# Performance work log

Measured on AMD Instinct MI355X. Metric: run time of the kernel, lower is better.

The kernel has to match this reference:

```python
import jax, jax.numpy as jnp
import numpy as np

ALPHA = 4.0   # spikingjelly surrogate.Sigmoid default alpha
TAU = 2.0
HEADS = 8

@jax.custom_vjp
def spike_fn(x):
    return (x >= 0).astype(x.dtype)

def _spike_fwd(x):
    return spike_fn(x), x

def _spike_bwd(x, g):
    s = jax.nn.sigmoid(ALPHA * x)
    return (g * ALPHA * s * (1.0 - s),)

spike_fn.defvjp(_spike_fwd, _spike_bwd)

def lif(x, v_th=1.0):
    """Multi-step LIF over leading time axis. Hard reset to 0, detach_reset."""
    def step(v, xt):
        v = v + (xt - v) / TAU
        s = spike_fn(v - v_th)
        v = v * (1.0 - jax.lax.stop_gradient(s))
        return v, s
    _, spikes = jax.lax.scan(step, jnp.zeros_like(x[0]), x)
    return spikes

def conv1x1(x, w, b=None):
    # x: (T,B,C,H,W), w: (O,C) -> (T,B,O,H,W)
    y = jnp.einsum('tbchw,oc->tbohw', x, w)
    if b is not None:
        y = y + b[None, None, :, None, None]
    return y

def bn(x, gamma, beta, mean, var, eps=1e-5):
    inv = gamma / jnp.sqrt(var + eps)
    shift = beta - mean * inv
    return x * inv[None, None, :, None, None] + shift[None, None, :, None, None]

def setup_inputs() -> dict:
    key = jax.random.key(0)
    T, B, C, H, W = 4, 16, 512, 16, 16
    ks = jax.random.split(key, 24)
    def w(k):
        return jax.random.normal(k, (C, C), jnp.float32) * (1.0 / np.sqrt(C))
    def bn_params(k0, k1):
        g = 1.0 + 0.1 * jax.random.normal(k0, (C,), jnp.float32)
        b = 0.1 * jax.random.normal(k1, (C,), jnp.float32)
        m = 0.1 * jax.random.normal(jax.random.fold_in(k0, 7), (C,), jnp.float32)
        v = jax.random.uniform(jax.random.fold_in(k1, 7), (C,), jnp.float32, 0.5, 1.5)
        return g, b, m, v
    x = jax.random.normal(ks[0], (T, B, C, H, W), jnp.float32)
    q_g, q_b, q_m, q_v = bn_params(ks[4], ks[5])
    k_g, k_b, k_m, k_v = bn_params(ks[6], ks[7])
    v_g, v_b, v_m, v_v = bn_params(ks[8], ks[9])
    p_g, p_b2, p_m, p_v = bn_params(ks[10], ks[11])
    return {
        'x': x,
        'q_w': w(ks[1]), 'q_g': q_g, 'q_b': q_b, 'q_m': q_m, 'q_v': q_v,
        'k_w': w(ks[2]), 'k_g': k_g, 'k_b': k_b, 'k_m': k_m, 'k_v': k_v,
        'v_w': w(ks[3]), 'v_g': v_g, 'v_b': v_b, 'v_m': v_m, 'v_v': v_v,
        'proj_w': w(ks[12]),
        'proj_b': 0.1 * jax.random.normal(ks[13], (C,), jnp.float32),
        'p_g': p_g, 'p_b2': p_b2, 'p_m': p_m, 'p_v': p_v,
    }

def reference(x, q_w, q_g, q_b, q_m, q_v, k_w, k_g, k_b, k_m, k_v,
              v_w, v_g, v_b, v_m, v_v, proj_w, proj_b, p_g, p_b2, p_m, p_v):
    T, B, C, H, W = x.shape
    d = C // HEADS
    N = H * W
    identity = x
    xs = lif(x)  # shortcut_lif

    def to_heads(y):
        # (T,B,C,H,W) -> flatten(3) -> (T,B,C,N) -> (T,B,N,C) -> (T,B,N,h,d) -> (T,B,h,N,d)
        return y.reshape(T, B, C, N).transpose(0, 1, 3, 2).reshape(T, B, N, HEADS, d).transpose(0, 1, 3, 2, 4)

    q = to_heads(lif(bn(conv1x1(xs, q_w), q_g, q_b, q_m, q_v)))
    k = to_heads(lif(bn(conv1x1(xs, k_w), k_g, k_b, k_m, k_v)))
    v = to_heads(lif(bn(conv1x1(xs, v_w), v_g, v_b, v_m, v_v)))

    kv = (k * v).sum(axis=3, keepdims=True)        # (T,B,h,1,d) linear spike attention
    kv = lif(kv, v_th=0.5)                         # talking_heads_lif (conv1d never applied in source forward)
    attn = q * kv                                  # (T,B,h,N,d)

    y = attn.transpose(0, 1, 2, 4, 3).reshape(T, B, C, H, W)
    y = bn(conv1x1(y, proj_w, proj_b), p_g, p_b2, p_m, p_v)
    return y + identity
```

## Files before the change

kernel.cpp:

```cpp
#include <hip/hip_runtime.h>


#define T_  4
#define B_  16
#define C_  512
#define N_  256
#define O3_ 1536
#define EPS_ 1e-5f

typedef unsigned int uint32;

__global__ void k0_prep(const float* __restrict__ qw, const float* __restrict__ kw,
                        const float* __restrict__ vw, const float* __restrict__ pw,
                        const float* qg,const float* qb,const float* qm,const float* qv,
                        const float* kg,const float* kb,const float* km,const float* kvr,
                        const float* vg,const float* vb,const float* vm,const float* vv,
                        const float* pg,const float* pb2,const float* pm,const float* pv,
                        const float* projb,
                        float* __restrict__ wqkv_t, float* __restrict__ pwt,
                        float* __restrict__ bnc){
    __shared__ float tile[64 * 65];
    int bx = blockIdx.x, tid = threadIdx.x;
    if (bx < 256) {
        const float* src; float* dst; int ocol;
        int tl;
        if (bx < 192) { int g = bx / 64; tl = bx % 64;
            src = (g == 0) ? qw : (g == 1) ? kw : vw;
            dst = wqkv_t; ocol = g * 512;
        } else { tl = bx - 192; src = pw; dst = pwt; ocol = 0; }
        int o0 = (tl >> 3) * 64, c0 = (tl & 7) * 64;
        int dstride = (bx < 192) ? O3_ : C_;
        #pragma unroll
        for (int i = 0; i < 16; i++) {
            int idx = i * 256 + tid;
            int cl = idx & 63, ol = idx >> 6;
            tile[ol * 65 + cl] = src[(size_t)(o0 + ol) * C_ + c0 + cl];
        }
        __syncthreads();
        #pragma unroll
        for (int i = 0; i < 16; i++) {
            int idx = i * 256 + tid;
            int ol = idx & 63, cl = idx >> 6;
            dst[(size_t)(c0 + cl) * dstride + ocol + o0 + ol] = tile[ol * 65 + cl];
        }
    } else {
        int ch = (bx - 256) * 256 + tid;
        if (ch < C_) {
            {   float inv = qg[ch] / sqrtf(qv[ch] + EPS_);
                bnc[ch] = inv;            bnc[512 + ch]  = qb[ch] - qm[ch] * inv; }
            {   float inv = kg[ch] / sqrtf(kvr[ch] + EPS_);
                bnc[1024 + ch] = inv;     bnc[1536 + ch] = kb[ch] - km[ch] * inv; }
            {   float inv = vg[ch] / sqrtf(vv[ch] + EPS_);
                bnc[2048 + ch] = inv;     bnc[2560 + ch] = vb[ch] - vm[ch] * inv; }
            {   float inv = pg[ch] / sqrtf(pv[ch] + EPS_);
                float shift = pb2[ch] - pm[ch] * inv;
                bnc[3072 + ch] = inv;     bnc[3584 + ch] = projb[ch] * inv + shift; }
        }
    }
}

__global__ void k1_lif_x(const float* __restrict__ x, uint32* __restrict__ xs_mask32){
    __shared__ uint32 sm32[64 * 17];
    int b = blockIdx.x, c0 = blockIdx.y * 64, n0 = blockIdx.z * 64;
    int tid = threadIdx.x;
    #pragma unroll
    for (int i = 0; i < 4; i++) {
        int idx = i * 256 + tid;
        int nq = idx & 15, cl = idx >> 4;
        const float* xp = x + ((size_t)b * C_ + c0 + cl) * N_ + n0 + nq * 4;
        float4 xv[4];
        #pragma unroll
        for (int t = 0; t < 4; t++)
            xv[t] = *reinterpret_cast<const float4*>(xp + (size_t)t * B_ * C_ * N_);
        uint32 packed = 0;
        #pragma unroll
        for (int e = 0; e < 4; e++) {
            float v = 0.f; unsigned m = 0;
            #pragma unroll
            for (int t = 0; t < 4; t++) {
                float xt = reinterpret_cast<const float*>(&xv[t])[e];
                v = v + (xt - v) * 0.5f;
                if (v - 1.0f >= 0.f) { m |= 1u << t; v = 0.f; }
            }
            packed |= m << (8 * e);
        }
        sm32[cl * 17 + nq] = packed;
    }
    __syncthreads();
    #pragma unroll
    for (int i = 0; i < 4; i++) {
        int idx = i * 256 + tid;
        int cq = idx & 15, nl = idx >> 4;
        uint32 outp = 0;
        #pragma unroll
        for (int e = 0; e < 4; e++) {
            uint32 wv = sm32[(cq * 4 + e) * 17 + (nl >> 2)];
            outp |= ((wv >> (8 * (nl & 3))) & 0xffu) << (8 * e);
        }
        xs_mask32[((size_t)b * N_ + n0 + nl) * 128 + (c0 >> 2) + cq] = outp;
    }
}

__global__ __launch_bounds__(384) void
k2_qkv(const unsigned char* __restrict__ xs_mask,
       const float* __restrict__ wqkv_t,
       const float* __restrict__ bnc,
       unsigned char* __restrict__ q_mask,
       unsigned char* __restrict__ kvand_mask){
    __shared__ uint32 smask[128];
    __shared__ uint32 scnt;
    __shared__ uint32 slist[512];
    int n = blockIdx.x, b = blockIdx.y, tid = threadIdx.x;
    size_t colbase = ((size_t)b * N_ + n) * C_;
    if (tid < 128) smask[tid] = reinterpret_cast<const uint32*>(xs_mask + colbase)[tid];
    if (tid == 0) scnt = 0;
    __syncthreads();
    if (tid < 256) {
        const unsigned char* smb = (const unsigned char*)smask;
        #pragma unroll
        for (int h = 0; h < 2; h++) {
            int c = tid + (h << 8);
            unsigned m = smb[c];
            if (m) { unsigned p = atomicAdd(&scnt, 1u); slist[p] = (unsigned)c | (m << 16); }
        }
    }
    __syncthreads();
    int cnt = scnt;

    int g = tid >> 7;
    float acc[4][4];
    #pragma unroll
    for (int t = 0; t < 4; t++)
        #pragma unroll
        for (int i = 0; i < 4; i++) acc[t][i] = 0.f;

#define ACC4(t, w_) { acc[t][0]+=w_.x; acc[t][1]+=w_.y; acc[t][2]+=w_.z; acc[t][3]+=w_.w; }
    int j = 0;
    for (; j + 4 <= cnt; j += 4) {
        unsigned e0 = __builtin_amdgcn_readfirstlane(slist[j]);
        unsigned e1 = __builtin_amdgcn_readfirstlane(slist[j + 1]);
        unsigned e2 = __builtin_amdgcn_readfirstlane(slist[j + 2]);
        unsigned e3 = __builtin_amdgcn_readfirstlane(slist[j + 3]);
        float4 w0 = reinterpret_cast<const float4*>(wqkv_t + (size_t)(e0 & 0xffffu) * O3_)[tid];
        float4 w1 = reinterpret_cast<const float4*>(wqkv_t + (size_t)(e1 & 0xffffu) * O3_)[tid];
        float4 w2 = reinterpret_cast<const float4*>(wqkv_t + (size_t)(e2 & 0xffffu) * O3_)[tid];
        float4 w3 = reinterpret_cast<const float4*>(wqkv_t + (size_t)(e3 & 0xffffu) * O3_)[tid];
        unsigned m0 = e0 >> 16, m1 = e1 >> 16, m2 = e2 >> 16, m3 = e3 >> 16;
        if (m0 & 1u) ACC4(0, w0)  if (m0 & 2u) ACC4(1, w0)
        if (m0 & 4u) ACC4(2, w0)  if (m0 & 8u) ACC4(3, w0)
        if (m1 & 1u) ACC4(0, w1)  if (m1 & 2u) ACC4(1, w1)
        if (m1 & 4u) ACC4(2, w1)  if (m1 & 8u) ACC4(3, w1)
        if (m2 & 1u) ACC4(0, w2)  if (m2 & 2u) ACC4(1, w2)
        if (m2 & 4u) ACC4(2, w2)  if (m2 & 8u) ACC4(3, w2)
        if (m3 & 1u) ACC4(0, w3)  if (m3 & 2u) ACC4(1, w3)
        if (m3 & 4u) ACC4(2, w3)  if (m3 & 8u) ACC4(3, w3)
    }
    for (; j < cnt; j++) {
        unsigned e0 = __builtin_amdgcn_readfirstlane(slist[j]);
        float4 w0 = reinterpret_cast<const float4*>(wqkv_t + (size_t)(e0 & 0xffffu) * O3_)[tid];
        unsigned m0 = e0 >> 16;
        if (m0 & 1u) ACC4(0, w0)  if (m0 & 2u) ACC4(1, w0)
        if (m0 & 4u) ACC4(2, w0)  if (m0 & 8u) ACC4(3, w0)
    }
#undef ACC4

    int chb = (tid & 127) * 4;
    unsigned packed = 0;
    #pragma unroll
    for (int i = 0; i < 4; i++) {
        int ch = chb + i;
        float inv = bnc[g * 1024 + ch];
        float sh  = bnc[g * 1024 + 512 + ch];
        float v = 0.f; unsigned bits = 0;
        #pragma unroll
        for (int t = 0; t < 4; t++) {
            float pre = acc[t][i] * inv + sh;
            v = v + (pre - v) * 0.5f;
            if (v - 1.0f >= 0.f) { bits |= 1u << t; v = 0.f; }
        }
        packed |= bits << (8 * i);
    }
    if (g == 0)      reinterpret_cast<uint32*>(q_mask + colbase)[tid] = packed;
    else if (g == 1) smask[tid - 128] = packed;
    __syncthreads();
    if (g == 2) {
        unsigned kb = smask[tid - 256];
        reinterpret_cast<uint32*>(kvand_mask + colbase)[tid - 256] = packed & kb;
    }
}

__global__ void k3_kv(const uint32* __restrict__ kvand32,
                      unsigned char* __restrict__ kvs_mask){
    __shared__ uint32 part[4][128];
    int b = blockIdx.x, tid = threadIdx.x;
    int c4 = tid & 127, sub = tid >> 7;
    const uint32* p = kvand32 + (size_t)b * N_ * 128 + (size_t)sub * 128 * 128 + c4;
    uint32 cnt0 = 0, cnt1 = 0, cnt2 = 0, cnt3 = 0;
    for (int i = 0; i < 128; i++) {
        uint32 m = p[(size_t)i * 128];
        cnt0 +=  m        & 0x01010101u;
        cnt1 += (m >> 1)  & 0x01010101u;
        cnt2 += (m >> 2)  & 0x01010101u;
        cnt3 += (m >> 3)  & 0x01010101u;
    }
    if (sub == 1) { part[0][c4] = cnt0; part[1][c4] = cnt1; part[2][c4] = cnt2; part[3][c4] = cnt3; }
    __syncthreads();
    if (sub == 0) {
        uint32 o0 = part[0][c4], o1 = part[1][c4], o2 = part[2][c4], o3 = part[3][c4];
        unsigned outp = 0;
        #pragma unroll
        for (int e = 0; e < 4; e++) {
            int sh = 8 * e;
            float cn[4];
            cn[0] = (float)(int)(((cnt0 >> sh) & 0xffu) + ((o0 >> sh) & 0xffu));
            cn[1] = (float)(int)(((cnt1 >> sh) & 0xffu) + ((o1 >> sh) & 0xffu));
            cn[2] = (float)(int)(((cnt2 >> sh) & 0xffu) + ((o2 >> sh) & 0xffu));
            cn[3] = (float)(int)(((cnt3 >> sh) & 0xffu) + ((o3 >> sh) & 0xffu));
            float v = 0.f; unsigned bits = 0;
            #pragma unroll
            for (int t = 0; t < 4; t++) {
                v = v + (cn[t] - v) * 0.5f;
                if (v - 0.5f >= 0.f) { bits |= 1u << t; v = 0.f; }
            }
            outp |= bits << sh;
        }
        reinterpret_cast<uint32*>(kvs_mask + (size_t)b * C_)[c4] = outp;
    }
}

__global__ __launch_bounds__(256) void
k4_attn_proj(const unsigned char* __restrict__ q_mask,
             const unsigned char* __restrict__ kvs_mask,
             const float* __restrict__ pwt,
             const float* __restrict__ bnc,
             float* __restrict__ y_t){
    __shared__ uint32 smask[2][128];
    __shared__ uint32 scnt[2];
    __shared__ uint32 slist[2][512];
    int b = blockIdx.y, tid = threadIdx.x;
    int col = tid >> 7, ctid = tid & 127;
    int n = blockIdx.x * 2 + col;
    size_t colbase = ((size_t)b * N_ + n) * C_;
    {
        uint32 qm = reinterpret_cast<const uint32*>(q_mask + colbase)[ctid];
        uint32 kv = reinterpret_cast<const uint32*>(kvs_mask + (size_t)b * C_)[ctid];
        smask[col][ctid] = qm & kv;
    }
    if (ctid == 0) scnt[col] = 0;
    __syncthreads();
    {
        const unsigned char* smb = (const unsigned char*)smask[col];
        #pragma unroll
        for (int h = 0; h < 4; h++) {
            int c = ctid * 4 + h;
            unsigned m = smb[c];
            if (m) { unsigned p = atomicAdd(&scnt[col], 1u); slist[col][p] = (unsigned)c | (m << 16); }
        }
    }
    __syncthreads();
    int cnt = scnt[col];
    const uint32* lst = slist[col];

    float acc[4][4];
    #pragma unroll
    for (int t = 0; t < 4; t++)
        #pragma unroll
        for (int i = 0; i < 4; i++) acc[t][i] = 0.f;

#define ACC4(t, w_) { acc[t][0]+=w_.x; acc[t][1]+=w_.y; acc[t][2]+=w_.z; acc[t][3]+=w_.w; }
    int j = 0;
    for (; j + 4 <= cnt; j += 4) {
        unsigned e0 = __builtin_amdgcn_readfirstlane(lst[j]);
        unsigned e1 = __builtin_amdgcn_readfirstlane(lst[j + 1]);
        unsigned e2 = __builtin_amdgcn_readfirstlane(lst[j + 2]);
        unsigned e3 = __builtin_amdgcn_readfirstlane(lst[j + 3]);
        float4 w0 = reinterpret_cast<const float4*>(pwt + (size_t)(e0 & 0xffffu) * C_)[ctid];
        float4 w1 = reinterpret_cast<const float4*>(pwt + (size_t)(e1 & 0xffffu) * C_)[ctid];
        float4 w2 = reinterpret_cast<const float4*>(pwt + (size_t)(e2 & 0xffffu) * C_)[ctid];
        float4 w3 = reinterpret_cast<const float4*>(pwt + (size_t)(e3 & 0xffffu) * C_)[ctid];
        unsigned m0 = e0 >> 16, m1 = e1 >> 16, m2 = e2 >> 16, m3 = e3 >> 16;
        if (m0 & 1u) ACC4(0, w0)  if (m0 & 2u) ACC4(1, w0)
        if (m0 & 4u) ACC4(2, w0)  if (m0 & 8u) ACC4(3, w0)
        if (m1 & 1u) ACC4(0, w1)  if (m1 & 2u) ACC4(1, w1)
        if (m1 & 4u) ACC4(2, w1)  if (m1 & 8u) ACC4(3, w1)
        if (m2 & 1u) ACC4(0, w2)  if (m2 & 2u) ACC4(1, w2)
        if (m2 & 4u) ACC4(2, w2)  if (m2 & 8u) ACC4(3, w2)
        if (m3 & 1u) ACC4(0, w3)  if (m3 & 2u) ACC4(1, w3)
        if (m3 & 4u) ACC4(2, w3)  if (m3 & 8u) ACC4(3, w3)
    }
    for (; j < cnt; j++) {
        unsigned e0 = __builtin_amdgcn_readfirstlane(lst[j]);
        float4 w0 = reinterpret_cast<const float4*>(pwt + (size_t)(e0 & 0xffffu) * C_)[ctid];
        unsigned m0 = e0 >> 16;
        if (m0 & 1u) ACC4(0, w0)  if (m0 & 2u) ACC4(1, w0)
        if (m0 & 4u) ACC4(2, w0)  if (m0 & 8u) ACC4(3, w0)
    }
#undef ACC4

    float4 inv = reinterpret_cast<const float4*>(bnc + 3072)[ctid];
    float4 sh  = reinterpret_cast<const float4*>(bnc + 3584)[ctid];
    #pragma unroll
    for (int t = 0; t < 4; t++) {
        float4 y4;
        y4.x = acc[t][0] * inv.x + sh.x;
        y4.y = acc[t][1] * inv.y + sh.y;
        y4.z = acc[t][2] * inv.z + sh.z;
        y4.w = acc[t][3] * inv.w + sh.w;
        reinterpret_cast<float4*>(y_t + (((size_t)t * B_ + b) * N_ + n) * C_)[ctid] = y4;
    }
}

__global__ void k5_out(const float* __restrict__ y_t, const float* __restrict__ x,
                       float* __restrict__ out){
    __shared__ float tile[64 * 65];
    int b = blockIdx.x, o0 = blockIdx.y * 64, n0 = blockIdx.z * 64;
    int tid = threadIdx.x;
    for (int t = 0; t < T_; t++) {
        __syncthreads();
        #pragma unroll
        for (int i = 0; i < 4; i++) {
            int idx = i * 256 + tid;
            int o4 = idx & 15, nl = idx >> 4;
            float4 yv = *reinterpret_cast<const float4*>(
                y_t + (((size_t)t * B_ + b) * N_ + n0 + nl) * C_ + o0 + o4 * 4);
            tile[(o4 * 4 + 0) * 65 + nl] = yv.x;
            tile[(o4 * 4 + 1) * 65 + nl] = yv.y;
            tile[(o4 * 4 + 2) * 65 + nl] = yv.z;
            tile[(o4 * 4 + 3) * 65 + nl] = yv.w;
        }
        __syncthreads();
        #pragma unroll
        for (int i = 0; i < 4; i++) {
            int idx = i * 256 + tid;
            int n4 = idx & 15, ol = idx >> 4;
            size_t a = (((size_t)t * B_ + b) * C_ + o0 + ol) * N_ + n0 + n4 * 4;
            float4 xv = *reinterpret_cast<const float4*>(x + a);
            float4 yv;
            yv.x = tile[ol * 65 + n4 * 4 + 0] + xv.x;
            yv.y = tile[ol * 65 + n4 * 4 + 1] + xv.y;
            yv.z = tile[ol * 65 + n4 * 4 + 2] + xv.z;
            yv.w = tile[ol * 65 + n4 * 4 + 3] + xv.w;
            *reinterpret_cast<float4*>(out + a) = yv;
        }
    }
}

extern "C" void kernel_launch(void* const* d_in, const int* in_sizes, int n_in,
                              void* d_out, int out_size, void* d_ws, size_t ws_size,
                              hipStream_t stream){
    const float* x     = (const float*)d_in[0];
    const float* q_w   = (const float*)d_in[1];
    const float* q_g   = (const float*)d_in[2];
    const float* q_b   = (const float*)d_in[3];
    const float* q_m   = (const float*)d_in[4];
    const float* q_v   = (const float*)d_in[5];
    const float* k_w   = (const float*)d_in[6];
    const float* k_g   = (const float*)d_in[7];
    const float* k_b   = (const float*)d_in[8];
    const float* k_m   = (const float*)d_in[9];
    const float* k_v   = (const float*)d_in[10];
    const float* v_w   = (const float*)d_in[11];
    const float* v_g   = (const float*)d_in[12];
    const float* v_b   = (const float*)d_in[13];
    const float* v_m   = (const float*)d_in[14];
    const float* v_v   = (const float*)d_in[15];
    const float* pr_w  = (const float*)d_in[16];
    const float* pr_b  = (const float*)d_in[17];
    const float* p_g   = (const float*)d_in[18];
    const float* p_b2  = (const float*)d_in[19];
    const float* p_m   = (const float*)d_in[20];
    const float* p_v   = (const float*)d_in[21];
    float* out = (float*)d_out;

    char* ws = (char*)d_ws;
    float* wqkv_t          = (float*)(ws + 0);
    float* pwt             = (float*)(ws + 3145728);
    float* bnc             = (float*)(ws + 4194304);
    unsigned char* xs_mask = (unsigned char*)(ws + 4210688);
    unsigned char* q_mask  = (unsigned char*)(ws + 6307840);
    unsigned char* kvand   = (unsigned char*)(ws + 8404992);
    unsigned char* kvs     = (unsigned char*)(ws + 10502144);
    float* y_t             = (float*)(ws + 10510336);

    hipLaunchKernelGGL(k0_prep, dim3(258), dim3(256), 0, stream,
                       q_w, k_w, v_w, pr_w,
                       q_g,q_b,q_m,q_v, k_g,k_b,k_m,k_v, v_g,v_b,v_m,v_v,
                       p_g,p_b2,p_m,p_v, pr_b, wqkv_t, pwt, bnc);
    hipLaunchKernelGGL(k1_lif_x, dim3(B_, C_/64, N_/64), dim3(256), 0, stream,
                       x, (uint32*)xs_mask);
    hipLaunchKernelGGL(k2_qkv, dim3(N_, B_), dim3(384), 0, stream,
                       xs_mask, wqkv_t, bnc, q_mask, kvand);
    hipLaunchKernelGGL(k3_kv, dim3(B_), dim3(256), 0, stream,
                       (const uint32*)kvand, kvs);
    hipLaunchKernelGGL(k4_attn_proj, dim3(N_/2, B_), dim3(256), 0, stream,
                       q_mask, kvs, pwt, bnc, y_t);
    hipLaunchKernelGGL(k5_out, dim3(B_, C_/64, N_/64), dim3(256), 0, stream, y_t, x, out);
}
```

Before: 212.4 us.

## Fold LIF-x into prep kernel and replace kv reduction kernel with atomics

Merges the input-LIF spike packing into the weight-prep kernel and adds blocks that zero a per-batch count buffer. The separate k3 reduction over the k&v spike masks is removed. k2 now atomically accumulates packed 16-bit per-channel counts into global memory, and k4 recomputes the talking-heads LIF from those counts. This cuts two launches and the round trip of the kvand mask, at the cost of global atomic contention in k2 and redundant LIF work in every k4 block.

```diff
diff --git a/kernel.cpp b/kernel.cpp
--- a/kernel.cpp
+++ b/kernel.cpp
@@ -10,16 +10,18 @@
 
 typedef unsigned int uint32;
 
-__global__ void k0_prep(const float* __restrict__ qw, const float* __restrict__ kw,
-                        const float* __restrict__ vw, const float* __restrict__ pw,
-                        const float* qg,const float* qb,const float* qm,const float* qv,
-                        const float* kg,const float* kb,const float* km,const float* kvr,
-                        const float* vg,const float* vb,const float* vm,const float* vv,
-                        const float* pg,const float* pb2,const float* pm,const float* pv,
-                        const float* projb,
-                        float* __restrict__ wqkv_t, float* __restrict__ pwt,
-                        float* __restrict__ bnc){
+__global__ void k_prep(const float* __restrict__ qw, const float* __restrict__ kw,
+                       const float* __restrict__ vw, const float* __restrict__ pw,
+                       const float* qg,const float* qb,const float* qm,const float* qv,
+                       const float* kg,const float* kb,const float* km,const float* kvr,
+                       const float* vg,const float* vb,const float* vm,const float* vv,
+                       const float* pg,const float* pb2,const float* pm,const float* pv,
+                       const float* projb, const float* __restrict__ x,
+                       float* __restrict__ wqkv_t, float* __restrict__ pwt,
+                       float* __restrict__ bnc, uint32* __restrict__ xs_mask32,
+                       uint32* __restrict__ cnt32){
     __shared__ float tile[64 * 65];
+    __shared__ uint32 sm32[64 * 17];
     int bx = blockIdx.x, tid = threadIdx.x;
     if (bx < 256) {
         const float* src; float* dst; int ocol;
@@ -43,7 +45,7 @@
             int ol = idx & 63, cl = idx >> 6;
             dst[(size_t)(c0 + cl) * dstride + ocol + o0 + ol] = tile[ol * 65 + cl];
         }
-    } else {
+    } else if (bx < 258) {
         int ch = (bx - 256) * 256 + tid;
         if (ch < C_) {
             {   float inv = qg[ch] / sqrtf(qv[ch] + EPS_);
@@ -56,48 +58,49 @@
                 float shift = pb2[ch] - pm[ch] * inv;
                 bnc[3072 + ch] = inv;     bnc[3584 + ch] = projb[ch] * inv + shift; }
         }
-    }
-}
-
-__global__ void k1_lif_x(const float* __restrict__ x, uint32* __restrict__ xs_mask32){
-    __shared__ uint32 sm32[64 * 17];
-    int b = blockIdx.x, c0 = blockIdx.y * 64, n0 = blockIdx.z * 64;
-    int tid = threadIdx.x;
-    #pragma unroll
-    for (int i = 0; i < 4; i++) {
-        int idx = i * 256 + tid;
-        int nq = idx & 15, cl = idx >> 4;
-        const float* xp = x + ((size_t)b * C_ + c0 + cl) * N_ + n0 + nq * 4;
-        float4 xv[4];
-        #pragma unroll
-        for (int t = 0; t < 4; t++)
-            xv[t] = *reinterpret_cast<const float4*>(xp + (size_t)t * B_ * C_ * N_);
-        uint32 packed = 0;
-        #pragma unroll
-        for (int e = 0; e < 4; e++) {
-            float v = 0.f; unsigned m = 0;
-            #pragma unroll
-            for (int t = 0; t < 4; t++) {
-                float xt = reinterpret_cast<const float*>(&xv[t])[e];
-                v = v + (xt - v) * 0.5f;
-                if (v - 1.0f >= 0.f) { m |= 1u << t; v = 0.f; }
+    } else if (bx < 770) {
+        int r = bx - 258;
+        int b = r >> 5, rem = r & 31;
+        int c0 = (rem >> 2) * 64, n0 = (rem & 3) * 64;
+        #pragma unroll
+        for (int i = 0; i < 4; i++) {
+            int idx = i * 256 + tid;
+            int nq = idx & 15, cl = idx >> 4;
+            const float* xp = x + ((size_t)b * C_ + c0 + cl) * N_ + n0 + nq * 4;
+            float4 xv[4];
+            #pragma unroll
+            for (int t = 0; t < 4; t++)
+                xv[t] = *reinterpret_cast<const float4*>(xp + (size_t)t * B_ * C_ * N_);
+            uint32 packed = 0;
+            #pragma unroll
+            for (int e = 0; e < 4; e++) {
+                float v = 0.f; unsigned m = 0;
+                #pragma unroll
+                for (int t = 0; t < 4; t++) {
+                    float xt = reinterpret_cast<const float*>(&xv[t])[e];
+                    v = v + (xt - v) * 0.5f;
+                    if (v - 1.0f >= 0.f) { m |= 1u << t; v = 0.f; }
+                }
+                packed |= m << (8 * e);
             }
-            packed |= m << (8 * e);
-        }
-        sm32[cl * 17 + nq] = packed;
-    }
-    __syncthreads();
-    #pragma unroll
-    for (int i = 0; i < 4; i++) {
-        int idx = i * 256 + tid;
-        int cq = idx & 15, nl = idx >> 4;
-        uint32 outp = 0;
-        #pragma unroll
-        for (int e = 0; e < 4; e++) {
-            uint32 wv = sm32[(cq * 4 + e) * 17 + (nl >> 2)];
-            outp |= ((wv >> (8 * (nl & 3))) & 0xffu) << (8 * e);
-        }
-        xs_mask32[((size_t)b * N_ + n0 + nl) * 128 + (c0 >> 2) + cq] = outp;
+            sm32[cl * 17 + nq] = packed;
+        }
+        __syncthreads();
+        #pragma unroll
+        for (int i = 0; i < 4; i++) {
+            int idx = i * 256 + tid;
+            int cq = idx & 15, nl = idx >> 4;
+            uint32 outp = 0;
+            #pragma unroll
+            for (int e = 0; e < 4; e++) {
+                uint32 wv = sm32[(cq * 4 + e) * 17 + (nl >> 2)];
+                outp |= ((wv >> (8 * (nl & 3))) & 0xffu) << (8 * e);
+            }
+            xs_mask32[((size_t)b * N_ + n0 + nl) * 128 + (c0 >> 2) + cq] = outp;
+        }
+    } else {
+        int idx = (bx - 770) * 256 + tid;
+        cnt32[idx] = 0;
     }
 }
 
@@ -106,7 +109,7 @@
        const float* __restrict__ wqkv_t,
        const float* __restrict__ bnc,
        unsigned char* __restrict__ q_mask,
-       unsigned char* __restrict__ kvand_mask){
+       uint32* __restrict__ cnt32){
     __shared__ uint32 smask[128];
     __shared__ uint32 scnt;
     __shared__ uint32 slist[512];
@@ -185,52 +188,23 @@
     __syncthreads();
     if (g == 2) {
         unsigned kb = smask[tid - 256];
-        reinterpret_cast<uint32*>(kvand_mask + colbase)[tid - 256] = packed & kb;
-    }
-}
-
-__global__ void k3_kv(const uint32* __restrict__ kvand32,
-                      unsigned char* __restrict__ kvs_mask){
-    __shared__ uint32 part[4][128];
-    int b = blockIdx.x, tid = threadIdx.x;
-    int c4 = tid & 127, sub = tid >> 7;
-    const uint32* p = kvand32 + (size_t)b * N_ * 128 + (size_t)sub * 128 * 128 + c4;
-    uint32 cnt0 = 0, cnt1 = 0, cnt2 = 0, cnt3 = 0;
-    for (int i = 0; i < 128; i++) {
-        uint32 m = p[(size_t)i * 128];
-        cnt0 +=  m        & 0x01010101u;
-        cnt1 += (m >> 1)  & 0x01010101u;
-        cnt2 += (m >> 2)  & 0x01010101u;
-        cnt3 += (m >> 3)  & 0x01010101u;
-    }
-    if (sub == 1) { part[0][c4] = cnt0; part[1][c4] = cnt1; part[2][c4] = cnt2; part[3][c4] = cnt3; }
-    __syncthreads();
-    if (sub == 0) {
-        uint32 o0 = part[0][c4], o1 = part[1][c4], o2 = part[2][c4], o3 = part[3][c4];
-        unsigned outp = 0;
-        #pragma unroll
-        for (int e = 0; e < 4; e++) {
-            int sh = 8 * e;
-            float cn[4];
-            cn[0] = (float)(int)(((cnt0 >> sh) & 0xffu) + ((o0 >> sh) & 0xffu));
-            cn[1] = (float)(int)(((cnt1 >> sh) & 0xffu) + ((o1 >> sh) & 0xffu));
-            cn[2] = (float)(int)(((cnt2 >> sh) & 0xffu) + ((o2 >> sh) & 0xffu));
-            cn[3] = (float)(int)(((cnt3 >> sh) & 0xffu) + ((o3 >> sh) & 0xffu));
-            float v = 0.f; unsigned bits = 0;
+        unsigned kv = packed & kb;
+        if (kv) {
+            uint32* cbase = cnt32 + b * 1024 + (chb >> 1);
             #pragma unroll
             for (int t = 0; t < 4; t++) {
-                v = v + (cn[t] - v) * 0.5f;
-                if (v - 0.5f >= 0.f) { bits |= 1u << t; v = 0.f; }
+                unsigned v01 = ((kv >> t) & 1u) | (((kv >> (8 + t)) & 1u) << 16);
+                unsigned v23 = ((kv >> (16 + t)) & 1u) | (((kv >> (24 + t)) & 1u) << 16);
+                if (v01) atomicAdd(cbase + t * 256, v01);
+                if (v23) atomicAdd(cbase + t * 256 + 1, v23);
             }
-            outp |= bits << sh;
-        }
-        reinterpret_cast<uint32*>(kvs_mask + (size_t)b * C_)[c4] = outp;
+        }
     }
 }
 
 __global__ __launch_bounds__(256) void
 k4_attn_proj(const unsigned char* __restrict__ q_mask,
-             const unsigned char* __restrict__ kvs_mask,
+             const uint32* __restrict__ cnt32,
              const float* __restrict__ pwt,
              const float* __restrict__ bnc,
              float* __restrict__ y_t){
@@ -241,10 +215,28 @@
     int col = tid >> 7, ctid = tid & 127;
     int n = blockIdx.x * 2 + col;
     size_t colbase = ((size_t)b * N_ + n) * C_;
+    unsigned kvs_packed = 0;
+    {
+        const uint32* cbase = cnt32 + b * 1024 + ctid * 2;
+        uint32 c01[4], c23[4];
+        #pragma unroll
+        for (int t = 0; t < 4; t++) { c01[t] = cbase[t * 256]; c23[t] = cbase[t * 256 + 1]; }
+        #pragma unroll
+        for (int e = 0; e < 4; e++) {
+            float v = 0.f; unsigned bits = 0;
+            #pragma unroll
+            for (int t = 0; t < 4; t++) {
+                uint32 pair = (e < 2) ? c01[t] : c23[t];
+                float cn = (float)(int)((e & 1) ? (pair >> 16) : (pair & 0xffffu));
+                v = v + (cn - v) * 0.5f;
+                if (v - 0.5f >= 0.f) { bits |= 1u << t; v = 0.f; }
+            }
+            kvs_packed |= bits << (8 * e);
+        }
+    }
     {
         uint32 qm = reinterpret_cast<const uint32*>(q_mask + colbase)[ctid];
-        uint32 kv = reinterpret_cast<const uint32*>(kvs_mask + (size_t)b * C_)[ctid];
-        smask[col][ctid] = qm & kv;
+        smask[col][ctid] = qm & kvs_packed;
     }
     if (ctid == 0) scnt[col] = 0;
     __syncthreads();
@@ -378,21 +370,17 @@
     float* bnc             = (float*)(ws + 4194304);
     unsigned char* xs_mask = (unsigned char*)(ws + 4210688);
     unsigned char* q_mask  = (unsigned char*)(ws + 6307840);
-    unsigned char* kvand   = (unsigned char*)(ws + 8404992);
-    unsigned char* kvs     = (unsigned char*)(ws + 10502144);
-    float* y_t             = (float*)(ws + 10510336);
-
-    hipLaunchKernelGGL(k0_prep, dim3(258), dim3(256), 0, stream,
+    uint32* cnt32          = (uint32*)(ws + 8404992);
+    float* y_t             = (float*)(ws + 8421376);
+
+    hipLaunchKernelGGL(k_prep, dim3(786), dim3(256), 0, stream,
                        q_w, k_w, v_w, pr_w,
                        q_g,q_b,q_m,q_v, k_g,k_b,k_m,k_v, v_g,v_b,v_m,v_v,
-                       p_g,p_b2,p_m,p_v, pr_b, wqkv_t, pwt, bnc);
-    hipLaunchKernelGGL(k1_lif_x, dim3(B_, C_/64, N_/64), dim3(256), 0, stream,
-                       x, (uint32*)xs_mask);
+                       p_g,p_b2,p_m,p_v, pr_b, x,
+                       wqkv_t, pwt, bnc, (uint32*)xs_mask, cnt32);
     hipLaunchKernelGGL(k2_qkv, dim3(N_, B_), dim3(384), 0, stream,
-                       xs_mask, wqkv_t, bnc, q_mask, kvand);
-    hipLaunchKernelGGL(k3_kv, dim3(B_), dim3(256), 0, stream,
-                       (const uint32*)kvand, kvs);
+                       xs_mask, wqkv_t, bnc, q_mask, cnt32);
     hipLaunchKernelGGL(k4_attn_proj, dim3(N_/2, B_), dim3(256), 0, stream,
-                       q_mask, kvs, pwt, bnc, y_t);
+                       q_mask, cnt32, pwt, bnc, y_t);
     hipLaunchKernelGGL(k5_out, dim3(B_, C_/64, N_/64), dim3(256), 0, stream, y_t, x, out);
 }
```

Measured after the change: 202.1 us. 1.05x faster.
